# Performance work log

Hardware: AMD Instinct MI355X
Metric: run time of the kernel (lower is better)

## Reference

```python
import jax, jax.numpy as jnp
import numpy as np

N_HOST, N_FLOW, E = 20000, 200000, 600000
D_IN, D_H, D_OUT = 64, 128, 32
NEG_SLOPE = 0.01  # F.leaky_relu default


def setup_inputs() -> dict:
    key = jax.random.key(0)
    ks = jax.random.split(key, 20)

    def w(k, shape):
        # kaiming-uniform-ish init scale (matches Linear fan-in scaling)
        lim = 1.0 / np.sqrt(shape[0])
        return jax.random.uniform(k, shape, jnp.float32, -lim, lim)

    return {
        "x_host": jax.random.normal(ks[0], (N_HOST, D_IN), jnp.float32),
        "x_flow": jax.random.normal(ks[1], (N_FLOW, D_IN), jnp.float32),
        "src_hf": jax.random.randint(ks[2], (E,), 0, N_HOST, dtype=jnp.int32),
        "dst_hf": jax.random.randint(ks[3], (E,), 0, N_FLOW, dtype=jnp.int32),
        "src_fh": jax.random.randint(ks[4], (E,), 0, N_FLOW, dtype=jnp.int32),
        "dst_fh": jax.random.randint(ks[5], (E,), 0, N_HOST, dtype=jnp.int32),
        "W0_hf_l": w(ks[6], (D_IN, D_H)), "W0_hf_r": w(ks[7], (D_IN, D_H)),
        "b0_hf": jnp.zeros((D_H,), jnp.float32),
        "W0_fh_l": w(ks[8], (D_IN, D_H)), "W0_fh_r": w(ks[9], (D_IN, D_H)),
        "b0_fh": jnp.zeros((D_H,), jnp.float32),
        "W1_hf_l": w(ks[10], (D_H, D_H)), "W1_hf_r": w(ks[11], (D_H, D_H)),
        "b1_hf": jnp.zeros((D_H,), jnp.float32),
        "W1_fh_l": w(ks[12], (D_H, D_H)), "W1_fh_r": w(ks[13], (D_H, D_H)),
        "b1_fh": jnp.zeros((D_H,), jnp.float32),
        "W_out": w(ks[14], (D_H, D_OUT)),
        "b_out": jnp.zeros((D_OUT,), jnp.float32),
    }


def _seg_mean(x, src, dst, n_dst):
    """Mean-aggregate src-node features over edges into n_dst segments."""
    s = jax.ops.segment_sum(x[src], dst, num_segments=n_dst)      # [n_dst, d]
    cnt = jax.ops.segment_sum(jnp.ones(src.shape, x.dtype), dst, num_segments=n_dst)
    return s / jnp.clip(cnt, 1.0)[:, None]


def _sage(x_src, x_dst, src, dst, Wl, Wr, b, n_dst):
    # SAGEConv: lin_l(mean_agg) + bias + lin_r(x_dst)
    agg = _seg_mean(x_src, src, dst, n_dst)
    return agg @ Wl + b + x_dst @ Wr


def reference(x_host, x_flow, src_hf, dst_hf, src_fh, dst_fh,
              W0_hf_l, W0_hf_r, b0_hf, W0_fh_l, W0_fh_r, b0_fh,
              W1_hf_l, W1_hf_r, b1_hf, W1_fh_l, W1_fh_r, b1_fh,
              W_out, b_out):
    lrelu = lambda v: jnp.where(v > 0, v, NEG_SLOPE * v)

    # layer 0
    h_flow = lrelu(_sage(x_host, x_flow, src_hf, dst_hf, W0_hf_l, W0_hf_r, b0_hf, N_FLOW))
    h_host = lrelu(_sage(x_flow, x_host, src_fh, dst_fh, W0_fh_l, W0_fh_r, b0_fh, N_HOST))

    # layer 1
    g_flow = lrelu(_sage(h_host, h_flow, src_hf, dst_hf, W1_hf_l, W1_hf_r, b1_hf, N_FLOW))
    g_host = lrelu(_sage(h_flow, h_host, src_fh, dst_fh, W1_fh_l, W1_fh_r, b1_fh, N_HOST))
    del g_host  # computed (matches module) but only 'flow' feeds the head

    return g_flow @ W_out + b_out  # [N_FLOW, D_OUT]
```

## Files before the change

kernel.cpp:

```cpp
#include <hip/hip_runtime.h>


#define N_HOST 20000
#define N_FLOW 200000
#define NEDGE  600000
#define D_IN   64
#define D_H    128
#define D_OUT  32
#define NSEG   (N_FLOW + N_HOST)
#define NBKT_F 196
#define NBKT_H 79
#define NBKT   (NBKT_F + NBKT_H)
#define NEB    586

typedef unsigned short u16;
typedef unsigned int   u32;
typedef short bf16x8 __attribute__((ext_vector_type(8)));
typedef float f32x4  __attribute__((ext_vector_type(4)));

__device__ __forceinline__ float bfh(u16 h) { return __uint_as_float(((u32)h) << 16); }
__device__ __forceinline__ u16 fbh(float f) {
    u32 u = __float_as_uint(f);
    return (u16)((u + 0x7fffu + ((u >> 16) & 1u)) >> 16);
}
__device__ __forceinline__ u32 packbf(float x, float y) {
    return (u32)fbh(x) | ((u32)fbh(y) << 16);
}
__device__ __forceinline__ void acc8(float* a, uint4 u) {
    a[0] += __uint_as_float(u.x << 16);
    a[1] += __uint_as_float(u.x & 0xffff0000u);
    a[2] += __uint_as_float(u.y << 16);
    a[3] += __uint_as_float(u.y & 0xffff0000u);
    a[4] += __uint_as_float(u.z << 16);
    a[5] += __uint_as_float(u.z & 0xffff0000u);
    a[6] += __uint_as_float(u.w << 16);
    a[7] += __uint_as_float(u.w & 0xffff0000u);
}

template <int W>
__device__ __forceinline__ uint4 gather_mean(const u16* __restrict__ pool, int rs, int coff,
                                             const int* __restrict__ csr, int st, int en) {
    float a[8] = {0.f, 0.f, 0.f, 0.f, 0.f, 0.f, 0.f, 0.f};
    for (int e = st; e < en; e += W) {
        uint4 u[W];
#pragma unroll
        for (int j = 0; j < W; j++) u[j] = make_uint4(0u, 0u, 0u, 0u);
#pragma unroll
        for (int j = 0; j < W; j++) {
            if (e + j < en) {
                int n = csr[e + j];
                u[j] = *(const uint4*)(pool + n * rs + coff);
            }
        }
#pragma unroll
        for (int j = 0; j < W; j++) acc8(a, u[j]);
    }
    float inv = (en > st) ? 1.f / (float)(en - st) : 0.f;
    uint4 o;
    o.x = packbf(a[0] * inv, a[1] * inv);
    o.y = packbf(a[2] * inv, a[3] * inv);
    o.z = packbf(a[4] * inv, a[5] * inv);
    o.w = packbf(a[6] * inv, a[7] * inv);
    return o;
}

__global__ void k_prep(const float* __restrict__ W0_hf_l, const float* __restrict__ W0_hf_r,
                       const float* __restrict__ W0_fh_l, const float* __restrict__ W0_fh_r,
                       const float* __restrict__ W1_l, const float* __restrict__ W1_r,
                       const float* __restrict__ Wout,
                       u16* __restrict__ WT0_hf, u16* __restrict__ WT0_fh,
                       u16* __restrict__ WT1_l, u16* __restrict__ WT1_r,
                       u16* __restrict__ WTo) {
    int b = blockIdx.x, t = threadIdx.x;
    u16 tmp[8];
    if (b < 32) {
        int e = (b & 7) * 2048 + t * 8;
        int n = e >> 7, k0 = e & 127;
        if (b < 8) {
#pragma unroll
            for (int j = 0; j < 8; j++) {
                int k = k0 + j;
                tmp[j] = fbh(k < 64 ? W0_hf_l[k * D_H + n] : W0_hf_r[(k - 64) * D_H + n]);
            }
            *(uint4*)(WT0_hf + n * 128 + k0) = *(uint4*)tmp;
        } else if (b < 16) {
#pragma unroll
            for (int j = 0; j < 8; j++) {
                int k = k0 + j;
                tmp[j] = fbh(k < 64 ? W0_fh_l[k * D_H + n] : W0_fh_r[(k - 64) * D_H + n]);
            }
            *(uint4*)(WT0_fh + n * 128 + k0) = *(uint4*)tmp;
        } else if (b < 24) {
#pragma unroll
            for (int j = 0; j < 8; j++) tmp[j] = fbh(W1_l[(k0 + j) * D_H + n]);
            *(uint4*)(WT1_l + n * 128 + k0) = *(uint4*)tmp;
        } else {
#pragma unroll
            for (int j = 0; j < 8; j++) tmp[j] = fbh(W1_r[(k0 + j) * D_H + n]);
            *(uint4*)(WT1_r + n * 128 + k0) = *(uint4*)tmp;
        }
    } else {
        int e = (b - 32) * 2048 + t * 8;
        int n = e >> 7, k0 = e & 127;
#pragma unroll
        for (int j = 0; j < 8; j++) tmp[j] = fbh(Wout[(k0 + j) * D_OUT + n]);
        *(uint4*)(WTo + n * 128 + k0) = *(uint4*)tmp;
    }
}

__global__ void k_cvt(const float* __restrict__ xf, const float* __restrict__ xh,
                      u16* __restrict__ xfb, u16* __restrict__ xhb) {
    int t = blockIdx.x * 256 + threadIdx.x;
    const int TF = (N_FLOW * D_IN) / 8;
    const int TT = TF + (N_HOST * D_IN) / 8;
    if (t >= TT) return;
    const float* src; u16* dst; int base;
    if (t < TF) { src = xf; dst = xfb; base = t * 8; }
    else        { src = xh; dst = xhb; base = (t - TF) * 8; }
    float4 f0 = *(const float4*)(src + base);
    float4 f1 = *(const float4*)(src + base + 4);
    uint4 o;
    o.x = packbf(f0.x, f0.y); o.y = packbf(f0.z, f0.w);
    o.z = packbf(f1.x, f1.y); o.w = packbf(f1.z, f1.w);
    *(uint4*)(dst + base) = o;
}

__device__ __forceinline__ int bucket_of(int combined_node) {
    return (combined_node < N_FLOW) ? (combined_node >> 10)
                                    : (NBKT_F + ((combined_node - N_FLOW) >> 8));
}

__global__ void kb1(const int* __restrict__ dst_hf, const int* __restrict__ dst_fh,
                    int* __restrict__ bcnt) {
    __shared__ int h[NBKT];
    int t = threadIdx.x;
    for (int j = t; j < NBKT; j += 256) h[j] = 0;
    __syncthreads();
    int base = blockIdx.x * 2048;
#pragma unroll
    for (int i = 0; i < 8; i++) {
        int e = base + t + i * 256;
        if (e < 2 * NEDGE) {
            int bkt = (e < NEDGE) ? (dst_hf[e] >> 10)
                                  : (NBKT_F + (dst_fh[e - NEDGE] >> 8));
            atomicAdd(&h[bkt], 1);
        }
    }
    __syncthreads();
    for (int j = t; j < NBKT; j += 256)
        if (h[j]) atomicAdd(&bcnt[j], h[j]);
}

__global__ void scanB(const int* __restrict__ bcnt, int* __restrict__ ebase) {
    __shared__ int sp[512];
    int t = threadIdx.x;
    int v = (t < NBKT) ? bcnt[t] : 0;
    sp[t] = v;
    __syncthreads();
    for (int d = 1; d < 512; d <<= 1) {
        int x = (t >= d) ? sp[t - d] : 0;
        __syncthreads();
        sp[t] += x;
        __syncthreads();
    }
    if (t < NBKT) ebase[t] = sp[t] - v;
    if (t == NBKT - 1) ebase[NBKT] = sp[t];
}

__global__ void kb2(const int* __restrict__ src_hf, const int* __restrict__ dst_hf,
                    const int* __restrict__ src_fh, const int* __restrict__ dst_fh,
                    const int* __restrict__ ebase, int* __restrict__ bcur,
                    int2* __restrict__ binE) {
    __shared__ int lh[NBKT];
    __shared__ int lb[NBKT];
    int t = threadIdx.x;
    for (int j = t; j < NBKT; j += 256) lh[j] = 0;
    __syncthreads();
    int base = blockIdx.x * 2048;
    int mybkt[8], myrank[8], mysrc[8], mydst[8];
#pragma unroll
    for (int i = 0; i < 8; i++) {
        int e = base + t + i * 256;
        mybkt[i] = -1;
        if (e < 2 * NEDGE) {
            int s, d;
            if (e < NEDGE) { s = src_hf[e]; d = dst_hf[e]; }
            else           { s = src_fh[e - NEDGE]; d = dst_fh[e - NEDGE] + N_FLOW; }
            int bkt = bucket_of(d);
            mybkt[i] = bkt; mysrc[i] = s; mydst[i] = d;
            myrank[i] = atomicAdd(&lh[bkt], 1);
        }
    }
    __syncthreads();
    for (int j = t; j < NBKT; j += 256)
        lb[j] = lh[j] ? atomicAdd(&bcur[j], lh[j]) : 0;
    __syncthreads();
#pragma unroll
    for (int i = 0; i < 8; i++) {
        if (mybkt[i] >= 0) {
            int pos = ebase[mybkt[i]] + lb[mybkt[i]] + myrank[i];
            binE[pos] = make_int2(mysrc[i], mydst[i]);
        }
    }
}

__global__ __launch_bounds__(256) void kb3(const int2* __restrict__ binE,
                                           const int* __restrict__ ebase,
                                           int* __restrict__ off, int* __restrict__ csr) {
    __shared__ int deg[1024];
    __shared__ int ts[256];
    int b = blockIdx.x, t = threadIdx.x;
    int nbase, ncnt;
    if (b < NBKT_F) { nbase = b << 10; ncnt = min(1024, N_FLOW - nbase); }
    else { nbase = N_FLOW + ((b - NBKT_F) << 8); ncnt = min(256, NSEG - nbase); }
    int e0 = ebase[b], e1 = ebase[b + 1];
    for (int i = t; i < 1024; i += 256) deg[i] = 0;
    __syncthreads();
    for (int e = e0 + t; e < e1; e += 256) {
        int2 p = binE[e];
        atomicAdd(&deg[p.y - nbase], 1);
    }
    __syncthreads();
    int loc[4]; int s = 0;
#pragma unroll
    for (int j = 0; j < 4; j++) { loc[j] = s; s += deg[t * 4 + j]; }
    ts[t] = s;
    __syncthreads();
    for (int d = 1; d < 256; d <<= 1) {
        int x = (t >= d) ? ts[t - d] : 0;
        __syncthreads();
        ts[t] += x;
        __syncthreads();
    }
    int base2 = e0 + ts[t] - s;
    int dsave[4];
#pragma unroll
    for (int j = 0; j < 4; j++) dsave[j] = deg[t * 4 + j];
    __syncthreads();
#pragma unroll
    for (int j = 0; j < 4; j++) {
        int idx = t * 4 + j;
        int st = base2 + loc[j];
        deg[idx] = st;
        if (idx < ncnt) off[nbase + idx] = st + dsave[j];
    }
    __syncthreads();
    for (int e = e0 + t; e < e1; e += 256) {
        int2 p = binE[e];
        int r = atomicAdd(&deg[p.y - nbase], 1);
        csr[r] = p.x;
    }
}

__global__ __launch_bounds__(256) void k_host(
    const u16* __restrict__ xfb, const u16* __restrict__ xhb,
    const int* __restrict__ off, const int* __restrict__ csr,
    const u16* __restrict__ WT0, const float* __restrict__ b0,
    const u16* __restrict__ WT1l, u16* __restrict__ hT, int M) {
    __shared__ __align__(16) u16 sA[64 * 136];
    const int t = threadIdx.x;
    const int m0 = blockIdx.x * 64;
#pragma unroll
    for (int i = 0; i < 2; i++) {
        int q = t + i * 256;
        int r = q >> 3, c = q & 7;
        int row = m0 + r;
        uint4 v = make_uint4(0u, 0u, 0u, 0u);
        if (row < M) v = *(const uint4*)(xhb + row * 64 + c * 8);
        *(uint4*)(&sA[r * 136 + 64 + c * 8]) = v;
    }
#pragma unroll
    for (int i = 0; i < 2; i++) {
        int q = t + i * 256;
        int r = q >> 3, c = q & 7;
        int row = m0 + r;
        uint4 o = make_uint4(0u, 0u, 0u, 0u);
        if (row < M) {
            int sid = N_FLOW + row;
            int st = off[sid - 1];
            int en = off[sid];
            o = gather_mean<8>(xfb, 64, c * 8, csr, st, en);
        }
        *(uint4*)(&sA[r * 136 + c * 8]) = o;
    }
    __syncthreads();
    const int w = t >> 6, ln = t & 63, l15 = ln & 15, quad = ln >> 4;
    const u16* pA = sA + (w * 16 + l15) * 136 + quad * 8;
    const u16* pB0 = WT0 + l15 * 128 + quad * 8;
    f32x4 acc[8];
#pragma unroll
    for (int tt = 0; tt < 8; tt++) acc[tt] = (f32x4){0.f, 0.f, 0.f, 0.f};
#pragma unroll
    for (int s = 0; s < 4; s++) {
        bf16x8 a = *(const bf16x8*)(pA + s * 32);
#pragma unroll
        for (int tt = 0; tt < 8; tt++) {
            bf16x8 b = *(const bf16x8*)(pB0 + tt * 2048 + s * 32);
            acc[tt] = __builtin_amdgcn_mfma_f32_16x16x32_bf16(a, b, acc[tt], 0, 0, 0);
        }
    }
#pragma unroll
    for (int tt = 0; tt < 8; tt++) {
        int col = tt * 16 + l15;
        float bv = b0[col];
#pragma unroll
        for (int i = 0; i < 4; i++) {
            int rl = w * 16 + quad * 4 + i;
            float v = acc[tt][i] + bv;
            v = v > 0.f ? v : 0.01f * v;
            sA[rl * 136 + col] = fbh(v);
        }
    }
    const u16* pB1 = WT1l + l15 * 128 + quad * 8;
    f32x4 accB[8];
#pragma unroll
    for (int tt = 0; tt < 8; tt++) accB[tt] = (f32x4){0.f, 0.f, 0.f, 0.f};
#pragma unroll
    for (int s = 0; s < 4; s++) {
        bf16x8 a = *(const bf16x8*)(pA + s * 32);
#pragma unroll
        for (int tt = 0; tt < 8; tt++) {
            bf16x8 b = *(const bf16x8*)(pB1 + tt * 2048 + s * 32);
            accB[tt] = __builtin_amdgcn_mfma_f32_16x16x32_bf16(a, b, accB[tt], 0, 0, 0);
        }
    }
#pragma unroll
    for (int tt = 0; tt < 8; tt++) {
        int col = tt * 16 + l15;
#pragma unroll
        for (int i = 0; i < 4; i++) {
            int row = m0 + w * 16 + quad * 4 + i;
            if (row < M) hT[row * D_H + col] = fbh(accB[tt][i]);
        }
    }
}

__global__ __launch_bounds__(256) void k_mega(
    const u16* __restrict__ xfb, const u16* __restrict__ xhb,
    const int* __restrict__ off, const int* __restrict__ csr,
    const u16* __restrict__ hT,
    const u16* __restrict__ WT0, const float* __restrict__ b0,
    const u16* __restrict__ WT1r, const float* __restrict__ b1,
    const u16* __restrict__ WTo, const float* __restrict__ bout,
    float* __restrict__ OUT) {
    __shared__ __align__(16) u16 sA[64 * 136];
    __shared__ __align__(16) u16 sAg[64 * 136];
    const int t = threadIdx.x;
    const int m0 = blockIdx.x * 64;
#pragma unroll
    for (int i = 0; i < 2; i++) {
        int q = t + i * 256;
        int r = q >> 3, c = q & 7;
        int row = m0 + r;
        uint4 v = *(const uint4*)(xfb + row * 64 + c * 8);
        *(uint4*)(&sA[r * 136 + 64 + c * 8]) = v;
    }
#pragma unroll
    for (int i = 0; i < 2; i++) {
        int q = t + i * 256;
        int r = q >> 3, c = q & 7;
        int row = m0 + r;
        int st = (row == 0) ? 0 : off[row - 1];
        int en = off[row];
        uint4 o = gather_mean<4>(xhb, 64, c * 8, csr, st, en);
        *(uint4*)(&sA[r * 136 + c * 8]) = o;
    }
#pragma unroll
    for (int i = 0; i < 4; i++) {
        int q = t + i * 256;
        int r = q >> 4, c = q & 15;
        int row = m0 + r;
        int st = (row == 0) ? 0 : off[row - 1];
        int en = off[row];
        uint4 o = gather_mean<4>(hT, 128, c * 8, csr, st, en);
        *(uint4*)(&sAg[r * 136 + c * 8]) = o;
    }
    __syncthreads();
    const int w = t >> 6, ln = t & 63, l15 = ln & 15, quad = ln >> 4;
    const u16* pA = sA + (w * 16 + l15) * 136 + quad * 8;
    const u16* pB0 = WT0 + l15 * 128 + quad * 8;
    f32x4 acc[8];
#pragma unroll
    for (int tt = 0; tt < 8; tt++) acc[tt] = (f32x4){0.f, 0.f, 0.f, 0.f};
#pragma unroll
    for (int s = 0; s < 4; s++) {
        bf16x8 a = *(const bf16x8*)(pA + s * 32);
#pragma unroll
        for (int tt = 0; tt < 8; tt++) {
            bf16x8 b = *(const bf16x8*)(pB0 + tt * 2048 + s * 32);
            acc[tt] = __builtin_amdgcn_mfma_f32_16x16x32_bf16(a, b, acc[tt], 0, 0, 0);
        }
    }
#pragma unroll
    for (int tt = 0; tt < 8; tt++) {
        int col = tt * 16 + l15;
        float bv = b0[col];
#pragma unroll
        for (int i = 0; i < 4; i++) {
            int rl = w * 16 + quad * 4 + i;
            float v = acc[tt][i] + bv;
            v = v > 0.f ? v : 0.01f * v;
            sA[rl * 136 + col] = fbh(v);
        }
    }
    const u16* pB1 = WT1r + l15 * 128 + quad * 8;
    f32x4 accB[8];
#pragma unroll
    for (int tt = 0; tt < 8; tt++) accB[tt] = (f32x4){0.f, 0.f, 0.f, 0.f};
#pragma unroll
    for (int s = 0; s < 4; s++) {
        bf16x8 a = *(const bf16x8*)(pA + s * 32);
#pragma unroll
        for (int tt = 0; tt < 8; tt++) {
            bf16x8 b = *(const bf16x8*)(pB1 + tt * 2048 + s * 32);
            accB[tt] = __builtin_amdgcn_mfma_f32_16x16x32_bf16(a, b, accB[tt], 0, 0, 0);
        }
    }
#pragma unroll
    for (int tt = 0; tt < 8; tt++) {
        int col = tt * 16 + l15;
        float bv = b1[col];
#pragma unroll
        for (int i = 0; i < 4; i++) {
            int rl = w * 16 + quad * 4 + i;
            float v = accB[tt][i] + bfh(sAg[rl * 136 + col]) + bv;
            v = v > 0.f ? v : 0.01f * v;
            sA[rl * 136 + col] = fbh(v);
        }
    }
    const u16* pBo = WTo + l15 * 128 + quad * 8;
    f32x4 acc2[2];
    acc2[0] = (f32x4){0.f, 0.f, 0.f, 0.f};
    acc2[1] = (f32x4){0.f, 0.f, 0.f, 0.f};
#pragma unroll
    for (int s = 0; s < 4; s++) {
        bf16x8 g = *(const bf16x8*)(pA + s * 32);
        acc2[0] = __builtin_amdgcn_mfma_f32_16x16x32_bf16(g, *(const bf16x8*)(pBo + s * 32), acc2[0], 0, 0, 0);
        acc2[1] = __builtin_amdgcn_mfma_f32_16x16x32_bf16(g, *(const bf16x8*)(pBo + 2048 + s * 32), acc2[1], 0, 0, 0);
    }
#pragma unroll
    for (int tt = 0; tt < 2; tt++) {
        int col = tt * 16 + l15;
        float bv = bout[col];
#pragma unroll
        for (int i = 0; i < 4; i++) {
            int row = m0 + w * 16 + quad * 4 + i;
            OUT[row * D_OUT + col] = acc2[tt][i] + bv;
        }
    }
}

extern "C" void kernel_launch(void* const* d_in, const int* in_sizes, int n_in,
                              void* d_out, int out_size, void* d_ws, size_t ws_size,
                              hipStream_t stream) {
    const float* x_host  = (const float*)d_in[0];
    const float* x_flow  = (const float*)d_in[1];
    const int* src_hf  = (const int*)d_in[2];
    const int* dst_hf  = (const int*)d_in[3];
    const int* src_fh  = (const int*)d_in[4];
    const int* dst_fh  = (const int*)d_in[5];
    const float* W0_hf_l = (const float*)d_in[6];
    const float* W0_hf_r = (const float*)d_in[7];
    const float* b0_hf   = (const float*)d_in[8];
    const float* W0_fh_l = (const float*)d_in[9];
    const float* W0_fh_r = (const float*)d_in[10];
    const float* b0_fh   = (const float*)d_in[11];
    const float* W1_hf_l = (const float*)d_in[12];
    const float* W1_hf_r = (const float*)d_in[13];
    const float* b1_hf   = (const float*)d_in[14];
    const float* W_out   = (const float*)d_in[18];
    const float* b_out   = (const float*)d_in[19];
    float* out = (float*)d_out;

    char* ws = (char*)d_ws;
    int*  off    = (int*)(ws + 0);
    int*  csr    = (int*)(ws + 880000);
    u16*  hT     = (u16*)(ws + 5680000);
    u16*  xfb    = (u16*)(ws + 10800000);
    u16*  xhb    = (u16*)(ws + 36400000);
    int2* binE   = (int2*)(ws + 38960000);
    int*  bcnt   = (int*)(ws + 48560000);
    int*  bcur   = (int*)(ws + 48561280);
    int*  ebase  = (int*)(ws + 48562560);
    u16*  WT0_hf = (u16*)(ws + 48563840);
    u16*  WT0_fh = (u16*)(ws + 48596608);
    u16*  WT1_l  = (u16*)(ws + 48629376);
    u16*  WT1_r  = (u16*)(ws + 48662144);
    u16*  WTo    = (u16*)(ws + 48694912);

    hipMemsetAsync(bcnt, 0, 2560, stream);
    k_prep<<<34, 256, 0, stream>>>(W0_hf_l, W0_hf_r, W0_fh_l, W0_fh_r, W1_hf_l, W1_hf_r,
                                   W_out, WT0_hf, WT0_fh, WT1_l, WT1_r, WTo);
    k_cvt<<<6875, 256, 0, stream>>>(x_flow, x_host, xfb, xhb);
    kb1<<<NEB, 256, 0, stream>>>(dst_hf, dst_fh, bcnt);
    scanB<<<1, 512, 0, stream>>>(bcnt, ebase);
    kb2<<<NEB, 256, 0, stream>>>(src_hf, dst_hf, src_fh, dst_fh, ebase, bcur, binE);
    kb3<<<NBKT, 256, 0, stream>>>(binE, ebase, off, csr);
    k_host<<<313, 256, 0, stream>>>(xfb, xhb, off, csr, WT0_fh, b0_fh, WT1_l, hT, N_HOST);
    k_mega<<<3125, 256, 0, stream>>>(xfb, xhb, off, csr, hT, WT0_hf, b0_hf,
                                     WT1_r, b1_hf, WTo, b_out, out);
}
```

Baseline: 401.6 us.

## Merge prep kernels, fold bucket scan into consumers, stage CSR windows in LDS

Folds the weight transpose, input bf16 conversion and bucket histogram into one launch. The single-block scan is removed and recomputed redundantly inside kb2 and kb3 blocks. The gather kernels now preload the block's offset range and, when it fits, the CSR index window into shared memory, so neighbour indices come from LDS instead of global memory. This cuts launch count and serial dependencies at the cost of repeated scans in every block and extra shared memory per block.

```diff
diff --git a/kernel.cpp b/kernel.cpp
--- a/kernel.cpp
+++ b/kernel.cpp
@@ -37,23 +37,23 @@
     a[7] += __uint_as_float(u.w & 0xffff0000u);
 }
 
-template <int W>
-__device__ __forceinline__ uint4 gather_mean(const u16* __restrict__ pool, int rs, int coff,
-                                             const int* __restrict__ csr, int st, int en) {
+__device__ __forceinline__ uint4 gmean(const u16* __restrict__ pool, int rs, int coff,
+                                       const int* __restrict__ gcsr,
+                                       const int* __restrict__ lcsr, int st0, bool fit,
+                                       int st, int en) {
     float a[8] = {0.f, 0.f, 0.f, 0.f, 0.f, 0.f, 0.f, 0.f};
-    for (int e = st; e < en; e += W) {
-        uint4 u[W];
-#pragma unroll
-        for (int j = 0; j < W; j++) u[j] = make_uint4(0u, 0u, 0u, 0u);
-#pragma unroll
-        for (int j = 0; j < W; j++) {
-            if (e + j < en) {
-                int n = csr[e + j];
-                u[j] = *(const uint4*)(pool + n * rs + coff);
-            }
-        }
-#pragma unroll
-        for (int j = 0; j < W; j++) acc8(a, u[j]);
+    for (int e = st; e < en; e += 4) {
+        int n[4];
+#pragma unroll
+        for (int j = 0; j < 4; j++)
+            n[j] = (e + j < en) ? (fit ? lcsr[e + j - st0] : gcsr[e + j]) : -1;
+        uint4 u[4];
+#pragma unroll
+        for (int j = 0; j < 4; j++)
+            u[j] = (n[j] >= 0) ? *(const uint4*)(pool + n[j] * rs + coff)
+                               : make_uint4(0u, 0u, 0u, 0u);
+#pragma unroll
+        for (int j = 0; j < 4; j++) acc8(a, u[j]);
     }
     float inv = (en > st) ? 1.f / (float)(en - st) : 0.f;
     uint4 o;
@@ -64,117 +64,108 @@
     return o;
 }
 
-__global__ void k_prep(const float* __restrict__ W0_hf_l, const float* __restrict__ W0_hf_r,
-                       const float* __restrict__ W0_fh_l, const float* __restrict__ W0_fh_r,
-                       const float* __restrict__ W1_l, const float* __restrict__ W1_r,
-                       const float* __restrict__ Wout,
-                       u16* __restrict__ WT0_hf, u16* __restrict__ WT0_fh,
-                       u16* __restrict__ WT1_l, u16* __restrict__ WT1_r,
-                       u16* __restrict__ WTo) {
+__global__ void k_pre(const float* __restrict__ W0_hf_l, const float* __restrict__ W0_hf_r,
+                      const float* __restrict__ W0_fh_l, const float* __restrict__ W0_fh_r,
+                      const float* __restrict__ W1_l, const float* __restrict__ W1_r,
+                      const float* __restrict__ Wout,
+                      u16* __restrict__ WT0_hf, u16* __restrict__ WT0_fh,
+                      u16* __restrict__ WT1_l, u16* __restrict__ WT1_r,
+                      u16* __restrict__ WTo,
+                      const float* __restrict__ xf, const float* __restrict__ xh,
+                      u16* __restrict__ xfb, u16* __restrict__ xhb,
+                      const int* __restrict__ dst_hf, const int* __restrict__ dst_fh,
+                      int* __restrict__ bcnt) {
     int b = blockIdx.x, t = threadIdx.x;
-    u16 tmp[8];
-    if (b < 32) {
-        int e = (b & 7) * 2048 + t * 8;
-        int n = e >> 7, k0 = e & 127;
-        if (b < 8) {
-#pragma unroll
-            for (int j = 0; j < 8; j++) {
-                int k = k0 + j;
-                tmp[j] = fbh(k < 64 ? W0_hf_l[k * D_H + n] : W0_hf_r[(k - 64) * D_H + n]);
+    if (b < 34) {
+        u16 tmp[8];
+        if (b < 32) {
+            int e = (b & 7) * 2048 + t * 8;
+            int n = e >> 7, k0 = e & 127;
+            if (b < 8) {
+#pragma unroll
+                for (int j = 0; j < 8; j++) {
+                    int k = k0 + j;
+                    tmp[j] = fbh(k < 64 ? W0_hf_l[k * D_H + n] : W0_hf_r[(k - 64) * D_H + n]);
+                }
+                *(uint4*)(WT0_hf + n * 128 + k0) = *(uint4*)tmp;
+            } else if (b < 16) {
+#pragma unroll
+                for (int j = 0; j < 8; j++) {
+                    int k = k0 + j;
+                    tmp[j] = fbh(k < 64 ? W0_fh_l[k * D_H + n] : W0_fh_r[(k - 64) * D_H + n]);
+                }
+                *(uint4*)(WT0_fh + n * 128 + k0) = *(uint4*)tmp;
+            } else if (b < 24) {
+#pragma unroll
+                for (int j = 0; j < 8; j++) tmp[j] = fbh(W1_l[(k0 + j) * D_H + n]);
+                *(uint4*)(WT1_l + n * 128 + k0) = *(uint4*)tmp;
+            } else {
+#pragma unroll
+                for (int j = 0; j < 8; j++) tmp[j] = fbh(W1_r[(k0 + j) * D_H + n]);
+                *(uint4*)(WT1_r + n * 128 + k0) = *(uint4*)tmp;
             }
-            *(uint4*)(WT0_hf + n * 128 + k0) = *(uint4*)tmp;
-        } else if (b < 16) {
-#pragma unroll
-            for (int j = 0; j < 8; j++) {
-                int k = k0 + j;
-                tmp[j] = fbh(k < 64 ? W0_fh_l[k * D_H + n] : W0_fh_r[(k - 64) * D_H + n]);
+        } else {
+            int e = (b - 32) * 2048 + t * 8;
+            int n = e >> 7, k0 = e & 127;
+#pragma unroll
+            for (int j = 0; j < 8; j++) tmp[j] = fbh(Wout[(k0 + j) * D_OUT + n]);
+            *(uint4*)(WTo + n * 128 + k0) = *(uint4*)tmp;
+        }
+    } else if (b < 34 + 6875) {
+        int q = (b - 34) * 256 + t;
+        const int TF = (N_FLOW * D_IN) / 8;
+        const int TT = TF + (N_HOST * D_IN) / 8;
+        if (q >= TT) return;
+        const float* src; u16* dst; int base;
+        if (q < TF) { src = xf; dst = xfb; base = q * 8; }
+        else        { src = xh; dst = xhb; base = (q - TF) * 8; }
+        float4 f0 = *(const float4*)(src + base);
+        float4 f1 = *(const float4*)(src + base + 4);
+        uint4 o;
+        o.x = packbf(f0.x, f0.y); o.y = packbf(f0.z, f0.w);
+        o.z = packbf(f1.x, f1.y); o.w = packbf(f1.z, f1.w);
+        *(uint4*)(dst + base) = o;
+    } else {
+        __shared__ int h[NBKT];
+        for (int j = t; j < NBKT; j += 256) h[j] = 0;
+        __syncthreads();
+        int base = (b - 34 - 6875) * 2048;
+#pragma unroll
+        for (int i = 0; i < 8; i++) {
+            int e = base + t + i * 256;
+            if (e < 2 * NEDGE) {
+                int bkt = (e < NEDGE) ? (dst_hf[e] >> 10)
+                                      : (NBKT_F + (dst_fh[e - NEDGE] >> 8));
+                atomicAdd(&h[bkt], 1);
             }
-            *(uint4*)(WT0_fh + n * 128 + k0) = *(uint4*)tmp;
-        } else if (b < 24) {
-#pragma unroll
-            for (int j = 0; j < 8; j++) tmp[j] = fbh(W1_l[(k0 + j) * D_H + n]);
-            *(uint4*)(WT1_l + n * 128 + k0) = *(uint4*)tmp;
-        } else {
-#pragma unroll
-            for (int j = 0; j < 8; j++) tmp[j] = fbh(W1_r[(k0 + j) * D_H + n]);
-            *(uint4*)(WT1_r + n * 128 + k0) = *(uint4*)tmp;
-        }
-    } else {
-        int e = (b - 32) * 2048 + t * 8;
-        int n = e >> 7, k0 = e & 127;
-#pragma unroll
-        for (int j = 0; j < 8; j++) tmp[j] = fbh(Wout[(k0 + j) * D_OUT + n]);
-        *(uint4*)(WTo + n * 128 + k0) = *(uint4*)tmp;
-    }
-}
-
-__global__ void k_cvt(const float* __restrict__ xf, const float* __restrict__ xh,
-                      u16* __restrict__ xfb, u16* __restrict__ xhb) {
-    int t = blockIdx.x * 256 + threadIdx.x;
-    const int TF = (N_FLOW * D_IN) / 8;
-    const int TT = TF + (N_HOST * D_IN) / 8;
-    if (t >= TT) return;
-    const float* src; u16* dst; int base;
-    if (t < TF) { src = xf; dst = xfb; base = t * 8; }
-    else        { src = xh; dst = xhb; base = (t - TF) * 8; }
-    float4 f0 = *(const float4*)(src + base);
-    float4 f1 = *(const float4*)(src + base + 4);
-    uint4 o;
-    o.x = packbf(f0.x, f0.y); o.y = packbf(f0.z, f0.w);
-    o.z = packbf(f1.x, f1.y); o.w = packbf(f1.z, f1.w);
-    *(uint4*)(dst + base) = o;
-}
-
-__device__ __forceinline__ int bucket_of(int combined_node) {
-    return (combined_node < N_FLOW) ? (combined_node >> 10)
-                                    : (NBKT_F + ((combined_node - N_FLOW) >> 8));
-}
-
-__global__ void kb1(const int* __restrict__ dst_hf, const int* __restrict__ dst_fh,
-                    int* __restrict__ bcnt) {
-    __shared__ int h[NBKT];
-    int t = threadIdx.x;
-    for (int j = t; j < NBKT; j += 256) h[j] = 0;
-    __syncthreads();
-    int base = blockIdx.x * 2048;
-#pragma unroll
-    for (int i = 0; i < 8; i++) {
-        int e = base + t + i * 256;
-        if (e < 2 * NEDGE) {
-            int bkt = (e < NEDGE) ? (dst_hf[e] >> 10)
-                                  : (NBKT_F + (dst_fh[e - NEDGE] >> 8));
-            atomicAdd(&h[bkt], 1);
-        }
-    }
-    __syncthreads();
-    for (int j = t; j < NBKT; j += 256)
-        if (h[j]) atomicAdd(&bcnt[j], h[j]);
-}
-
-__global__ void scanB(const int* __restrict__ bcnt, int* __restrict__ ebase) {
-    __shared__ int sp[512];
-    int t = threadIdx.x;
-    int v = (t < NBKT) ? bcnt[t] : 0;
-    sp[t] = v;
-    __syncthreads();
-    for (int d = 1; d < 512; d <<= 1) {
-        int x = (t >= d) ? sp[t - d] : 0;
-        __syncthreads();
-        sp[t] += x;
-        __syncthreads();
-    }
-    if (t < NBKT) ebase[t] = sp[t] - v;
-    if (t == NBKT - 1) ebase[NBKT] = sp[t];
+        }
+        __syncthreads();
+        for (int j = t; j < NBKT; j += 256)
+            if (h[j]) atomicAdd(&bcnt[j], h[j]);
+    }
 }
 
 __global__ void kb2(const int* __restrict__ src_hf, const int* __restrict__ dst_hf,
                     const int* __restrict__ src_fh, const int* __restrict__ dst_fh,
-                    const int* __restrict__ ebase, int* __restrict__ bcur,
+                    const int* __restrict__ bcnt, int* __restrict__ bcur,
                     int2* __restrict__ binE) {
+    __shared__ int sp[512];
     __shared__ int lh[NBKT];
     __shared__ int lb[NBKT];
     int t = threadIdx.x;
+    int o1 = (t < NBKT) ? bcnt[t] : 0;
+    int o2 = (t + 256 < NBKT) ? bcnt[t + 256] : 0;
+    sp[t] = o1; sp[t + 256] = o2;
     for (int j = t; j < NBKT; j += 256) lh[j] = 0;
+    __syncthreads();
+    for (int d = 1; d < 512; d <<= 1) {
+        int a0 = (t >= d) ? sp[t - d] : 0;
+        int a1 = sp[t + 256 - d];
+        __syncthreads();
+        sp[t] += a0; sp[t + 256] += a1;
+        __syncthreads();
+    }
+    sp[t] -= o1; sp[t + 256] -= o2;
     __syncthreads();
     int base = blockIdx.x * 2048;
     int mybkt[8], myrank[8], mysrc[8], mydst[8];
@@ -186,7 +177,7 @@
             int s, d;
             if (e < NEDGE) { s = src_hf[e]; d = dst_hf[e]; }
             else           { s = src_fh[e - NEDGE]; d = dst_fh[e - NEDGE] + N_FLOW; }
-            int bkt = bucket_of(d);
+            int bkt = (d < N_FLOW) ? (d >> 10) : (NBKT_F + ((d - N_FLOW) >> 8));
             mybkt[i] = bkt; mysrc[i] = s; mydst[i] = d;
             myrank[i] = atomicAdd(&lh[bkt], 1);
         }
@@ -198,22 +189,34 @@
 #pragma unroll
     for (int i = 0; i < 8; i++) {
         if (mybkt[i] >= 0) {
-            int pos = ebase[mybkt[i]] + lb[mybkt[i]] + myrank[i];
+            int pos = sp[mybkt[i]] + lb[mybkt[i]] + myrank[i];
             binE[pos] = make_int2(mysrc[i], mydst[i]);
         }
     }
 }
 
 __global__ __launch_bounds__(256) void kb3(const int2* __restrict__ binE,
-                                           const int* __restrict__ ebase,
+                                           const int* __restrict__ bcnt,
                                            int* __restrict__ off, int* __restrict__ csr) {
+    __shared__ int sp[512];
     __shared__ int deg[1024];
     __shared__ int ts[256];
     int b = blockIdx.x, t = threadIdx.x;
+    sp[t] = (t < NBKT) ? bcnt[t] : 0;
+    sp[t + 256] = (t + 256 < NBKT) ? bcnt[t + 256] : 0;
+    __syncthreads();
+    for (int d = 1; d < 512; d <<= 1) {
+        int a0 = (t >= d) ? sp[t - d] : 0;
+        int a1 = sp[t + 256 - d];
+        __syncthreads();
+        sp[t] += a0; sp[t + 256] += a1;
+        __syncthreads();
+    }
+    int e0 = (b == 0) ? 0 : sp[b - 1];
+    int e1 = sp[b];
     int nbase, ncnt;
     if (b < NBKT_F) { nbase = b << 10; ncnt = min(1024, N_FLOW - nbase); }
     else { nbase = N_FLOW + ((b - NBKT_F) << 8); ncnt = min(256, NSEG - nbase); }
-    int e0 = ebase[b], e1 = ebase[b + 1];
     for (int i = t; i < 1024; i += 256) deg[i] = 0;
     __syncthreads();
     for (int e = e0 + t; e < e1; e += 256) {
@@ -258,8 +261,14 @@
     const u16* __restrict__ WT0, const float* __restrict__ b0,
     const u16* __restrict__ WT1l, u16* __restrict__ hT, int M) {
     __shared__ __align__(16) u16 sA[64 * 136];
+    __shared__ int sOff[72];
+    __shared__ int sCsr[2560];
     const int t = threadIdx.x;
     const int m0 = blockIdx.x * 64;
+    if (t < 65) {
+        int idx = N_FLOW + m0 - 1 + t;
+        sOff[t] = off[min(idx, NSEG - 1)];
+    }
 #pragma unroll
     for (int i = 0; i < 2; i++) {
         int q = t + i * 256;
@@ -269,18 +278,19 @@
         if (row < M) v = *(const uint4*)(xhb + row * 64 + c * 8);
         *(uint4*)(&sA[r * 136 + 64 + c * 8]) = v;
     }
+    __syncthreads();
+    int st0 = sOff[0];
+    int win = sOff[64] - st0;
+    bool fit = (win <= 2560);
+    if (fit) for (int e = t; e < win; e += 256) sCsr[e] = csr[st0 + e];
+    __syncthreads();
 #pragma unroll
     for (int i = 0; i < 2; i++) {
         int q = t + i * 256;
         int r = q >> 3, c = q & 7;
         int row = m0 + r;
         uint4 o = make_uint4(0u, 0u, 0u, 0u);
-        if (row < M) {
-            int sid = N_FLOW + row;
-            int st = off[sid - 1];
-            int en = off[sid];
-            o = gather_mean<8>(xfb, 64, c * 8, csr, st, en);
-        }
+        if (row < M) o = gmean(xfb, 64, c * 8, csr, sCsr, st0, fit, sOff[r], sOff[r + 1]);
         *(uint4*)(&sA[r * 136 + c * 8]) = o;
     }
     __syncthreads();
@@ -345,8 +355,14 @@
     float* __restrict__ OUT) {
     __shared__ __align__(16) u16 sA[64 * 136];
     __shared__ __align__(16) u16 sAg[64 * 136];
+    __shared__ int sOff[72];
+    __shared__ int sCsr[1024];
     const int t = threadIdx.x;
     const int m0 = blockIdx.x * 64;
+    if (t < 65) {
+        int idx = m0 - 1 + t;
+        sOff[t] = (idx < 0) ? 0 : off[idx];
+    }
 #pragma unroll
     for (int i = 0; i < 2; i++) {
         int q = t + i * 256;
@@ -355,24 +371,24 @@
         uint4 v = *(const uint4*)(xfb + row * 64 + c * 8);
         *(uint4*)(&sA[r * 136 + 64 + c * 8]) = v;
     }
+    __syncthreads();
+    int st0 = sOff[0];
+    int win = sOff[64] - st0;
+    bool fit = (win <= 1024);
+    if (fit) for (int e = t; e < win; e += 256) sCsr[e] = csr[st0 + e];
+    __syncthreads();
 #pragma unroll
     for (int i = 0; i < 2; i++) {
         int q = t + i * 256;
         int r = q >> 3, c = q & 7;
-        int row = m0 + r;
-        int st = (row == 0) ? 0 : off[row - 1];
-        int en = off[row];
-        uint4 o = gather_mean<4>(xhb, 64, c * 8, csr, st, en);
+        uint4 o = gmean(xhb, 64, c * 8, csr, sCsr, st0, fit, sOff[r], sOff[r + 1]);
         *(uint4*)(&sA[r * 136 + c * 8]) = o;
     }
 #pragma unroll
     for (int i = 0; i < 4; i++) {
         int q = t + i * 256;
         int r = q >> 4, c = q & 15;
-        int row = m0 + r;
-        int st = (row == 0) ? 0 : off[row - 1];
-        int en = off[row];
-        uint4 o = gather_mean<4>(hT, 128, c * 8, csr, st, en);
+        uint4 o = gmean(hT, 128, c * 8, csr, sCsr, st0, fit, sOff[r], sOff[r + 1]);
         *(uint4*)(&sAg[r * 136 + c * 8]) = o;
     }
     __syncthreads();
@@ -481,21 +497,19 @@
     int2* binE   = (int2*)(ws + 38960000);
     int*  bcnt   = (int*)(ws + 48560000);
     int*  bcur   = (int*)(ws + 48561280);
-    int*  ebase  = (int*)(ws + 48562560);
-    u16*  WT0_hf = (u16*)(ws + 48563840);
-    u16*  WT0_fh = (u16*)(ws + 48596608);
-    u16*  WT1_l  = (u16*)(ws + 48629376);
-    u16*  WT1_r  = (u16*)(ws + 48662144);
-    u16*  WTo    = (u16*)(ws + 48694912);
+    u16*  WT0_hf = (u16*)(ws + 48562560);
+    u16*  WT0_fh = (u16*)(ws + 48595328);
+    u16*  WT1_l  = (u16*)(ws + 48628096);
+    u16*  WT1_r  = (u16*)(ws + 48660864);
+    u16*  WTo    = (u16*)(ws + 48693632);
 
     hipMemsetAsync(bcnt, 0, 2560, stream);
-    k_prep<<<34, 256, 0, stream>>>(W0_hf_l, W0_hf_r, W0_fh_l, W0_fh_r, W1_hf_l, W1_hf_r,
-                                   W_out, WT0_hf, WT0_fh, WT1_l, WT1_r, WTo);
-    k_cvt<<<6875, 256, 0, stream>>>(x_flow, x_host, xfb, xhb);
-    kb1<<<NEB, 256, 0, stream>>>(dst_hf, dst_fh, bcnt);
-    scanB<<<1, 512, 0, stream>>>(bcnt, ebase);
-    kb2<<<NEB, 256, 0, stream>>>(src_hf, dst_hf, src_fh, dst_fh, ebase, bcur, binE);
-    kb3<<<NBKT, 256, 0, stream>>>(binE, ebase, off, csr);
+    k_pre<<<34 + 6875 + NEB, 256, 0, stream>>>(
+        W0_hf_l, W0_hf_r, W0_fh_l, W0_fh_r, W1_hf_l, W1_hf_r, W_out,
+        WT0_hf, WT0_fh, WT1_l, WT1_r, WTo,
+        x_flow, x_host, xfb, xhb, dst_hf, dst_fh, bcnt);
+    kb2<<<NEB, 256, 0, stream>>>(src_hf, dst_hf, src_fh, dst_fh, bcnt, bcur, binE);
+    kb3<<<NBKT, 256, 0, stream>>>(binE, bcnt, off, csr);
     k_host<<<313, 256, 0, stream>>>(xfb, xhb, off, csr, WT0_fh, b0_fh, WT1_l, hT, N_HOST);
     k_mega<<<3125, 256, 0, stream>>>(xfb, xhb, off, csr, hT, WT0_hf, b0_hf,
                                      WT1_r, b1_hf, WTo, b_out, out);
```

Measured after the change: 355.2 us. -11.6%, faster.
